# Performance work log

Measured on AMD Instinct MI355X. Metric: run time of the kernel, lower is better.

Reference implementation:

```python
import jax, jax.numpy as jnp
import numpy as np

B, A, NC, DIR, LMAX, MAXZ, NORB = 8, 64, 128, 4, 2, 10, 14
NF = NC * DIR * (2 * LMAX + 1)   # 2560
O2 = NORB * NORB                 # 196
AO = A * NORB                    # 896
LOG2 = float(np.log(2.0))

def ssp(v):  # spk shifted softplus
    return jax.nn.softplus(v) - LOG2

def setup_inputs():
    key = jax.random.key(0)
    ks = jax.random.split(key, 12)
    Z = jax.random.randint(ks[0], (B, A), 1, MAXZ)
    idx = np.arange(A)
    nbh_np = np.stack([np.delete(idx, i) for i in range(A)], 0)  # [A, A-1]: all atoms except self
    nbh = jnp.asarray(np.broadcast_to(nbh_np[None], (B, A, A - 1)).copy(), dtype=jnp.int32)
    x = jax.random.normal(ks[1], (B, A, NC), jnp.float32)
    Vijkl = jax.random.normal(ks[2], (B, A, A - 1, NF), jnp.float32) * 0.1
    sc = 1.0 / np.sqrt(NF)
    W_off = jax.random.normal(ks[3], (NF, O2), jnp.float32) * sc
    b_off = jnp.zeros((O2,), jnp.float32)
    W_on = jax.random.normal(ks[4], (NF, O2), jnp.float32) * sc
    b_on = jnp.zeros((O2,), jnp.float32)
    W_ovoff = jax.random.normal(ks[5], (NF, O2), jnp.float32) * sc
    b_ovoff = jnp.zeros((O2,), jnp.float32)
    ov_emb = jax.random.normal(ks[6], (MAXZ, O2), jnp.float32) * 0.1  # trainable overlap onsite embedding
    orb_energies = jax.random.normal(ks[7], (MAXZ, NORB), jnp.float32)  # h0 energies
    s0_energies = jnp.ones((MAXZ, NORB), jnp.float32)                   # s0 init = ones
    W1 = jax.random.normal(ks[8], (NC, NC // 2), jnp.float32) / np.sqrt(NC)
    b1 = jnp.zeros((NC // 2,), jnp.float32)
    W2 = jax.random.normal(ks[9], (NC // 2, 1), jnp.float32) / np.sqrt(NC // 2)
    b2 = jnp.zeros((1,), jnp.float32)
    return {"Z": Z, "nbh": nbh, "x": x, "Vijkl": Vijkl,
            "W_off": W_off, "b_off": b_off, "W_on": W_on, "b_on": b_on,
            "W_ovoff": W_ovoff, "b_ovoff": b_ovoff, "ov_emb": ov_emb,
            "orb_energies": orb_energies, "s0_energies": s0_energies,
            "W1": W1, "b1": b1, "W2": W2, "b2": b2}

def reference(Z, nbh, x, Vijkl, W_off, b_off, W_on, b_on, W_ovoff, b_ovoff,
              ov_emb, orb_energies, s0_energies, W1, b1, W2, b2):
    # permutation that reorders neighbor slots (plus appended zero/self slot) into atom order
    ar = jnp.broadcast_to(jnp.arange(A, dtype=nbh.dtype)[None, :, None], (B, A, 1))
    sort_idx = jnp.argsort(jnp.concatenate([nbh, ar], axis=2), axis=2)  # [B,A,A]
    eyeA = jnp.eye(A, dtype=Vijkl.dtype)
    eyeAO = jnp.eye(AO, dtype=Vijkl.dtype)

    def assemble(off, on):
        # off: [B,A,A-1,O2] pair blocks; on: [B,A,O2] onsite blocks
        offz = jnp.concatenate([off, jnp.zeros((B, A, 1, O2), off.dtype)], axis=2)  # zero self block at slot A-1
        offg = jnp.take_along_axis(offz, sort_idx[..., None], axis=2)               # [B,A,A,O2]
        M = offg + eyeA[None, :, :, None] * on[:, :, None, :]
        M = M.reshape(B, A, A, NORB, NORB).transpose(0, 1, 3, 2, 4).reshape(B, AO, AO)
        return 0.5 * (M + M.transpose(0, 2, 1))

    # Hamiltonian: offsite Dense + onsite Dense mean-aggregated over pairs
    H_off = Vijkl @ W_off + b_off                       # [B,A,A-1,O2]
    H_on = jnp.mean(Vijkl @ W_on + b_on, axis=2)        # [B,A,O2]
    H = assemble(H_off, H_on)
    # h0 single-atom diagonal (orb mask is all-active -> full diagonal)
    H = H + eyeAO[None] * orb_energies[Z].reshape(B, 1, AO)

    # Overlap: offsite Dense + onsite embedding lookup
    S_off = Vijkl @ W_ovoff + b_ovoff
    S_on = ov_emb[Z]                                    # [B,A,O2]
    S = assemble(S_off, S_on)
    S = S + eyeAO[None] * s0_energies[Z].reshape(B, 1, AO)

    # energy head: Dense->ssp->Dense->ScaleShift(0,1), sum over atoms
    Ei = ssp(x @ W1 + b1) @ W2 + b2                     # [B,A,1]
    E = jnp.sum(Ei, axis=1)                             # [B,1]
    return H, S, E
```

## Files before the change

### kernel.cpp

```cpp
#include <hip/hip_runtime.h>

#define B_      8
#define A_      64
#define NPAIR   63
#define NC_     128
#define NF_     2560
#define O2_     196
#define NORB_   14
#define AO_     896
#define NCOLS   588
#define CSTRIDE 640
#define KSTEPS  80
#define BM      64
#define BN      640
#define BSTEP_BYTES 40960

typedef short bf16x8 __attribute__((ext_vector_type(8)));
typedef float f32x4  __attribute__((ext_vector_type(4)));

__device__ __forceinline__ unsigned f2bf(float f) {
    unsigned u = __builtin_bit_cast(unsigned, f);
    return (u + 0x7fffu + ((u >> 16) & 1u)) >> 16;
}

__global__ __launch_bounds__(512)
void prep_energy(const float* __restrict__ W_off, const float* __restrict__ W_ovoff,
                 const float* __restrict__ W_on, unsigned short* __restrict__ Bws,
                 const float* __restrict__ x, const float* __restrict__ W1,
                 const float* __restrict__ b1, const float* __restrict__ W2,
                 const float* __restrict__ b2, float* __restrict__ E) {
    const int t = threadIdx.x;
    if (blockIdx.x < KSTEPS) {
        __shared__ float wt[32 * BN];
        const int ks = blockIdx.x;
        for (int e = t; e < 32 * BN; e += 512) {
            int kl = e / BN, c = e - kl * BN;
            int kg = ks * 32 + kl;
            float v = 0.f;
            if (c < O2_)          v = W_off  [(size_t)kg * O2_ + c];
            else if (c < 2 * O2_) v = W_ovoff[(size_t)kg * O2_ + (c - O2_)];
            else if (c < 3 * O2_) v = W_on   [(size_t)kg * O2_ + (c - 2 * O2_)];
            wt[kl * BN + c] = v;
        }
        __syncthreads();
        unsigned short* out = Bws + (size_t)ks * (BN * 32);
        for (int e = t; e < BN * 4; e += 512) {
            int n = e >> 2, sg = e & 3;
            uint4 w;
            w.x = f2bf(wt[(sg * 8 + 0) * BN + n]) | (f2bf(wt[(sg * 8 + 1) * BN + n]) << 16);
            w.y = f2bf(wt[(sg * 8 + 2) * BN + n]) | (f2bf(wt[(sg * 8 + 3) * BN + n]) << 16);
            w.z = f2bf(wt[(sg * 8 + 4) * BN + n]) | (f2bf(wt[(sg * 8 + 5) * BN + n]) << 16);
            w.w = f2bf(wt[(sg * 8 + 6) * BN + n]) | (f2bf(wt[(sg * 8 + 7) * BN + n]) << 16);
            *(uint4*)(out + (size_t)n * 32 + sg * 8) = w;
        }
    } else {
        __shared__ float partial[8];
        const int b = blockIdx.x - KSTEPS;
        const int lane = t & 63;
        const int w = t >> 6;
        float esum = 0.f;
        for (int aa = 0; aa < 8; ++aa) {
            const int a = w * 8 + aa;
            const float* xr = x + (size_t)(b * A_ + a) * NC_;
            float hj = b1[lane];
            for (int k = 0; k < NC_; ++k) hj = fmaf(xr[k], W1[k * 64 + lane], hj);
            float sp = fmaxf(hj, 0.f) + log1pf(expf(-fabsf(hj))) - 0.69314718055994531f;
            float v = sp * W2[lane];
            for (int off = 32; off; off >>= 1) v += __shfl_down(v, off);
            if (lane == 0) esum += v + b2[0];
        }
        if (lane == 0) partial[w] = esum;
        __syncthreads();
        if (t == 0) {
            float e = 0.f;
            for (int k = 0; k < 8; ++k) e += partial[k];
            E[b] = e;
        }
    }
}

__global__ __launch_bounds__(512, 4)
void gemm_off(const float* __restrict__ V, const unsigned short* __restrict__ Bws,
              const float* __restrict__ b_off, const float* __restrict__ b_ovoff,
              const float* __restrict__ b_on, float* __restrict__ HSoff) {
    __shared__ alignas(16) float Alds[2][BM * 32];

    const int tid  = threadIdx.x;
    int mtb = blockIdx.x;
    mtb = (mtb & 7) * 63 + (mtb >> 3);
    const int mt   = mtb;
    const int lane = tid & 63;
    const int wv   = tid >> 6;
    const int wvu  = __builtin_amdgcn_readfirstlane(wv);

    const int rr  = tid >> 3;
    const int sgp = (tid & 7) ^ (rr & 7);
    const float* asrc = V + (size_t)(mt * BM + rr) * NF_ + sgp * 4;

    const char* bp = (const char*)Bws + (size_t)(wv * 80 + (lane & 15)) * 64 + (lane >> 4) * 16;
#define BFRAG(t_, nf_) (*(const bf16x8*)(bp + (size_t)(t_) * BSTEP_BYTES + (nf_) * 1024))

    f32x4 acc[4][5];
#pragma unroll
    for (int mf = 0; mf < 4; ++mf)
#pragma unroll
        for (int nf = 0; nf < 5; ++nf)
            acc[mf][nf] = (f32x4){0.f, 0.f, 0.f, 0.f};

    auto stage = [&](int buf, int t) {
        __builtin_amdgcn_global_load_lds(
            (const __attribute__((address_space(1))) void*)(asrc + (size_t)t * 32),
            (__attribute__((address_space(3))) void*)(&Alds[buf][wvu * 256]), 16, 0, 0);
    };

    const unsigned klo = (unsigned)(lane >> 4) * 2;

    union U8 { unsigned u[4]; bf16x8 v; };

#define AFRAG(abf_, mf_, Abuf_) {                                                  \
    const unsigned R_ = (unsigned)(lane & 15) + (mf_) * 16;                        \
    const unsigned a0_ = R_ * 128 + ((klo ^ (R_ & 7)) << 4);                       \
    float4 lo_ = *(const float4*)((const char*)(Abuf_) + a0_);                     \
    float4 hi_ = *(const float4*)((const char*)(Abuf_) + (a0_ ^ 16));              \
    U8 uu_;                                                                        \
    asm("v_cvt_pk_bf16_f32 %0, %1, %2" : "=v"(uu_.u[0]) : "v"(lo_.x), "v"(lo_.y)); \
    asm("v_cvt_pk_bf16_f32 %0, %1, %2" : "=v"(uu_.u[1]) : "v"(lo_.z), "v"(lo_.w)); \
    asm("v_cvt_pk_bf16_f32 %0, %1, %2" : "=v"(uu_.u[2]) : "v"(hi_.x), "v"(hi_.y)); \
    asm("v_cvt_pk_bf16_f32 %0, %1, %2" : "=v"(uu_.u[3]) : "v"(hi_.z), "v"(hi_.w)); \
    abf_ = uu_.v; }

#define MFMA1(abf_, bq_, mf_, nf_) \
    acc[mf_][nf_] = __builtin_amdgcn_mfma_f32_16x16x32_bf16(abf_, bq_, acc[mf_][nf_], 0, 0, 0);

    bf16x8 bq0, bq1, bq2, bq3, bq4, abf;

    stage(0, 0);
    bq0 = BFRAG(0, 0); bq1 = BFRAG(0, 1); bq2 = BFRAG(0, 2); bq3 = BFRAG(0, 3); bq4 = BFRAG(0, 4);

    for (int t = 0; t < KSTEPS; ++t) {
        const int buf = t & 1;
        asm volatile("s_waitcnt vmcnt(5)" ::: "memory");
        __builtin_amdgcn_s_barrier();
        __builtin_amdgcn_sched_barrier(0);
        if (t + 1 < KSTEPS) stage(buf ^ 1, t + 1);

        const float* Abuf = &Alds[buf][0];
        AFRAG(abf, 0, Abuf);
        MFMA1(abf, bq0, 0, 0); MFMA1(abf, bq1, 0, 1); MFMA1(abf, bq2, 0, 2);
        MFMA1(abf, bq3, 0, 3); MFMA1(abf, bq4, 0, 4);
        AFRAG(abf, 1, Abuf);
        MFMA1(abf, bq0, 1, 0); MFMA1(abf, bq1, 1, 1); MFMA1(abf, bq2, 1, 2);
        MFMA1(abf, bq3, 1, 3); MFMA1(abf, bq4, 1, 4);
        AFRAG(abf, 2, Abuf);
        MFMA1(abf, bq0, 2, 0); MFMA1(abf, bq1, 2, 1); MFMA1(abf, bq2, 2, 2);
        MFMA1(abf, bq3, 2, 3); MFMA1(abf, bq4, 2, 4);
        AFRAG(abf, 3, Abuf);
        MFMA1(abf, bq0, 3, 0); bq0 = BFRAG(t + 1, 0);
        MFMA1(abf, bq1, 3, 1); bq1 = BFRAG(t + 1, 1);
        MFMA1(abf, bq2, 3, 2); bq2 = BFRAG(t + 1, 2);
        MFMA1(abf, bq3, 3, 3); bq3 = BFRAG(t + 1, 3);
        MFMA1(abf, bq4, 3, 4); bq4 = BFRAG(t + 1, 4);
        __builtin_amdgcn_sched_barrier(0);
    }

    const int c16 = lane & 15, rg = lane >> 4;
#pragma unroll
    for (int nf = 0; nf < 5; ++nf) {
        int C = wv * 80 + nf * 16 + c16;
        if (C >= NCOLS) continue;
        float bias = (C < O2_) ? b_off[C] : (C < 2 * O2_) ? b_ovoff[C - O2_] : b_on[C - 2 * O2_];
#pragma unroll
        for (int mf = 0; mf < 4; ++mf) {
            int R = mt * BM + mf * 16 + rg * 4;
            float* o = HSoff + (size_t)R * CSTRIDE + C;
            o[0]           = acc[mf][nf][0] + bias;
            o[CSTRIDE]     = acc[mf][nf][1] + bias;
            o[2 * CSTRIDE] = acc[mf][nf][2] + bias;
            o[3 * CSTRIDE] = acc[mf][nf][3] + bias;
        }
    }
#undef BFRAG
#undef AFRAG
#undef MFMA1
}

__global__ void hon_reduce(const float* __restrict__ HSoff, float* __restrict__ Hon) {
    const int g = blockIdx.x;
    const int t = threadIdx.x;
    if (t >= O2_) return;
    const float* p0 = HSoff + (size_t)g * NPAIR * CSTRIDE + 2 * O2_ + t;
    const float* p1 = p0 + (size_t)21 * CSTRIDE;
    const float* p2 = p0 + (size_t)42 * CSTRIDE;
    float a0 = 0.f, a1 = 0.f, a2 = 0.f;
#pragma unroll 3
    for (int j = 0; j < 21; ++j) {
        a0 += p0[0]; a1 += p1[0]; a2 += p2[0];
        p0 += CSTRIDE; p1 += CSTRIDE; p2 += CSTRIDE;
    }
    Hon[(size_t)g * O2_ + t] = (a0 + a1 + a2) * (1.f / (float)NPAIR);
}

__global__ __launch_bounds__(256)
void assemble_k(const float* __restrict__ HSoff, const float* __restrict__ Hon,
                const int* __restrict__ Z, const float* __restrict__ ov_emb,
                const float* __restrict__ orbE, const float* __restrict__ s0E,
                float* __restrict__ H, float* __restrict__ S) {
    __shared__ float Ai[NPAIR * 197];
    __shared__ float Bj[2][16 * 200];
    __shared__ float Dg[O2_];
    __shared__ float Dd[NORB_];

    const int bid = blockIdx.x;
    const int h = bid & 1, i = (bid >> 1) & 63, b = bid >> 7;
    const int t = threadIdx.x;
    const int g = b * A_ + i;
    const int z = Z[g];
    float* out = (h ? S : H) + (size_t)b * AO_ * AO_;

    const float* abase = HSoff + (size_t)g * NPAIR * CSTRIDE + h * O2_;
    for (int u = t; u < NPAIR * O2_; u += 256) {
        int jj = u / O2_, e = u - jj * O2_;
        Ai[jj * 197 + e] = abase[(size_t)jj * CSTRIDE + e];
    }
    if (t < O2_)   Dg[t] = h ? ov_emb[(size_t)z * O2_ + t]   : Hon[(size_t)g * O2_ + t];
    if (t < NORB_) Dd[t] = h ? s0E[(size_t)z * NORB_ + t]    : orbE[(size_t)z * NORB_ + t];

    auto stageB = [&](int buf, int jc) {
        for (int u = t; u < 16 * O2_; u += 256) {
            int jl = u / O2_, e = u - jl * O2_;
            int j = jc * 16 + jl;
            if (j != i) {
                int idx = (i < j) ? i : i - 1;
                Bj[buf][jl * 200 + e] =
                    HSoff[((size_t)(b * A_ + j) * NPAIR + idx) * CSTRIDE + h * O2_ + e];
            }
        }
    };
    stageB(0, 0);
    __syncthreads();

    const int tj = t / NORB_, tq = t - tj * NORB_;
    for (int jc = 0; jc < 4; ++jc) {
        if (jc < 3) stageB((jc + 1) & 1, jc + 1);
        if (t < 224) {
            const int j = jc * 16 + tj;
            const int cur = jc & 1;
#pragma unroll
            for (int p = 0; p < NORB_; ++p) {
                float v;
                if (j == i) {
                    v = 0.5f * (Dg[p * NORB_ + tq] + Dg[tq * NORB_ + p]);
                    if (p == tq) v += Dd[p];
                } else {
                    int jj = (j < i) ? j : j - 1;
                    v = 0.5f * (Ai[jj * 197 + p * NORB_ + tq] + Bj[cur][tj * 200 + tq * NORB_ + p]);
                }
                out[(size_t)(i * NORB_ + p) * AO_ + jc * 224 + t] = v;
            }
        }
        __syncthreads();
    }
}

extern "C" void kernel_launch(void* const* d_in, const int* in_sizes, int n_in,
                              void* d_out, int out_size, void* d_ws, size_t ws_size,
                              hipStream_t stream) {
    const int*   Z       = (const int*)  d_in[0];
    const float* x       = (const float*)d_in[2];
    const float* V       = (const float*)d_in[3];
    const float* W_off   = (const float*)d_in[4];
    const float* b_off   = (const float*)d_in[5];
    const float* W_on    = (const float*)d_in[6];
    const float* b_on    = (const float*)d_in[7];
    const float* W_ovoff = (const float*)d_in[8];
    const float* b_ovoff = (const float*)d_in[9];
    const float* ov_emb  = (const float*)d_in[10];
    const float* orbE    = (const float*)d_in[11];
    const float* s0E     = (const float*)d_in[12];
    const float* W1      = (const float*)d_in[13];
    const float* b1      = (const float*)d_in[14];
    const float* W2      = (const float*)d_in[15];
    const float* b2      = (const float*)d_in[16];

    float* H = (float*)d_out;
    float* S = H + (size_t)B_ * AO_ * AO_;
    float* E = S + (size_t)B_ * AO_ * AO_;

    char* ws = (char*)d_ws;
    unsigned short* Bws = (unsigned short*)ws;
    float* HSoff = (float*)(ws + (size_t)4  * 1024 * 1024);
    float* Hon   = (float*)(ws + (size_t)88 * 1024 * 1024);

    prep_energy<<<KSTEPS + B_, 512, 0, stream>>>(W_off, W_ovoff, W_on, Bws,
                                                 x, W1, b1, W2, b2, E);
    gemm_off   <<<504,  512, 0, stream>>>(V, Bws, b_off, b_ovoff, b_on, HSoff);
    hon_reduce <<<512,  256, 0, stream>>>(HSoff, Hon);
    assemble_k <<<1024, 256, 0, stream>>>(HSoff, Hon, Z, ov_emb, orbE, s0E, H, S);
}
```

Measured before the change: 265.9 us.

## Convert A tile to bf16 once per block in LDS before MFMA

Instead of every wave converting fp32 A fragments to bf16 on each read (8 waves each redoing the conversion), each thread converts one float4 of the staged tile into a separate bf16 LDS buffer with a new swizzle. MFMA fragments then come from a single 16-byte bf16 LDS load. The change adds an extra barrier and an lgkmcnt wait per k-step, plus more LDS use. It also wraps the MFMA groups in s_setprio to favour matrix issue.

```diff
diff --git a/kernel.cpp b/kernel.cpp
--- a/kernel.cpp
+++ b/kernel.cpp
@@ -83,7 +83,8 @@
 void gemm_off(const float* __restrict__ V, const unsigned short* __restrict__ Bws,
               const float* __restrict__ b_off, const float* __restrict__ b_ovoff,
               const float* __restrict__ b_on, float* __restrict__ HSoff) {
-    __shared__ alignas(16) float Alds[2][BM * 32];
+    __shared__ alignas(16) float          Af32[2][BM * 32];
+    __shared__ alignas(16) unsigned short Ab16[2][BM * 32];
 
     const int tid  = threadIdx.x;
     int mtb = blockIdx.x;
@@ -93,9 +94,7 @@
     const int wv   = tid >> 6;
     const int wvu  = __builtin_amdgcn_readfirstlane(wv);
 
-    const int rr  = tid >> 3;
-    const int sgp = (tid & 7) ^ (rr & 7);
-    const float* asrc = V + (size_t)(mt * BM + rr) * NF_ + sgp * 4;
+    const float* asrc = V + (size_t)(mt * BM + (tid >> 3)) * NF_ + (tid & 7) * 4;
 
     const char* bp = (const char*)Bws + (size_t)(wv * 80 + (lane & 15)) * 64 + (lane >> 4) * 16;
 #define BFRAG(t_, nf_) (*(const bf16x8*)(bp + (size_t)(t_) * BSTEP_BYTES + (nf_) * 1024))
@@ -110,24 +109,20 @@
     auto stage = [&](int buf, int t) {
         __builtin_amdgcn_global_load_lds(
             (const __attribute__((address_space(1))) void*)(asrc + (size_t)t * 32),
-            (__attribute__((address_space(3))) void*)(&Alds[buf][wvu * 256]), 16, 0, 0);
+            (__attribute__((address_space(3))) void*)(&Af32[buf][wvu * 256]), 16, 0, 0);
     };
 
-    const unsigned klo = (unsigned)(lane >> 4) * 2;
-
-    union U8 { unsigned u[4]; bf16x8 v; };
-
-#define AFRAG(abf_, mf_, Abuf_) {                                                  \
-    const unsigned R_ = (unsigned)(lane & 15) + (mf_) * 16;                        \
-    const unsigned a0_ = R_ * 128 + ((klo ^ (R_ & 7)) << 4);                       \
-    float4 lo_ = *(const float4*)((const char*)(Abuf_) + a0_);                     \
-    float4 hi_ = *(const float4*)((const char*)(Abuf_) + (a0_ ^ 16));              \
-    U8 uu_;                                                                        \
-    asm("v_cvt_pk_bf16_f32 %0, %1, %2" : "=v"(uu_.u[0]) : "v"(lo_.x), "v"(lo_.y)); \
-    asm("v_cvt_pk_bf16_f32 %0, %1, %2" : "=v"(uu_.u[1]) : "v"(lo_.z), "v"(lo_.w)); \
-    asm("v_cvt_pk_bf16_f32 %0, %1, %2" : "=v"(uu_.u[2]) : "v"(hi_.x), "v"(hi_.y)); \
-    asm("v_cvt_pk_bf16_f32 %0, %1, %2" : "=v"(uu_.u[3]) : "v"(hi_.z), "v"(hi_.w)); \
-    abf_ = uu_.v; }
+    const int crr = tid >> 3, cq = tid & 7;
+    const int csl = ((cq >> 1) + ((crr + (crr >> 2)) & 3)) & 3;
+    char* const cdst_base0 = (char*)&Ab16[0][0] + crr * 64 + csl * 16 + (cq & 1) * 8;
+    char* const cdst_base1 = (char*)&Ab16[1][0] + crr * 64 + csl * 16 + (cq & 1) * 8;
+
+    const unsigned klo4 = (unsigned)(lane >> 4);
+
+#define AFRAG(abf_, mf_, Bb16_) {                                                   \
+    const unsigned R_ = (unsigned)(lane & 15) + (mf_) * 16;                         \
+    const unsigned sl_ = (klo4 + ((R_ + (R_ >> 2)) & 3)) & 3;                       \
+    abf_ = *(const bf16x8*)((const char*)(Bb16_) + R_ * 64 + sl_ * 16); }
 
 #define MFMA1(abf_, bq_, mf_, nf_) \
     acc[mf_][nf_] = __builtin_amdgcn_mfma_f32_16x16x32_bf16(abf_, bq_, acc[mf_][nf_], 0, 0, 0);
@@ -140,26 +135,48 @@
     for (int t = 0; t < KSTEPS; ++t) {
         const int buf = t & 1;
         asm volatile("s_waitcnt vmcnt(5)" ::: "memory");
+        __builtin_amdgcn_sched_barrier(0);
         __builtin_amdgcn_s_barrier();
         __builtin_amdgcn_sched_barrier(0);
         if (t + 1 < KSTEPS) stage(buf ^ 1, t + 1);
 
-        const float* Abuf = &Alds[buf][0];
-        AFRAG(abf, 0, Abuf);
+        {
+            float4 cf = *(const float4*)((const char*)&Af32[buf][0] + tid * 16);
+            unsigned lo, hi;
+            asm("v_cvt_pk_bf16_f32 %0, %1, %2" : "=v"(lo) : "v"(cf.x), "v"(cf.y));
+            asm("v_cvt_pk_bf16_f32 %0, %1, %2" : "=v"(hi) : "v"(cf.z), "v"(cf.w));
+            uint2 cw = {lo, hi};
+            *(uint2*)(buf ? cdst_base1 : cdst_base0) = cw;
+        }
+        asm volatile("s_waitcnt lgkmcnt(0)" ::: "memory");
+        __builtin_amdgcn_sched_barrier(0);
+        __builtin_amdgcn_s_barrier();
+        __builtin_amdgcn_sched_barrier(0);
+
+        const unsigned short* At = &Ab16[buf][0];
+        AFRAG(abf, 0, At);
+        __builtin_amdgcn_s_setprio(1);
         MFMA1(abf, bq0, 0, 0); MFMA1(abf, bq1, 0, 1); MFMA1(abf, bq2, 0, 2);
         MFMA1(abf, bq3, 0, 3); MFMA1(abf, bq4, 0, 4);
-        AFRAG(abf, 1, Abuf);
+        __builtin_amdgcn_s_setprio(0);
+        AFRAG(abf, 1, At);
+        __builtin_amdgcn_s_setprio(1);
         MFMA1(abf, bq0, 1, 0); MFMA1(abf, bq1, 1, 1); MFMA1(abf, bq2, 1, 2);
         MFMA1(abf, bq3, 1, 3); MFMA1(abf, bq4, 1, 4);
-        AFRAG(abf, 2, Abuf);
+        __builtin_amdgcn_s_setprio(0);
+        AFRAG(abf, 2, At);
+        __builtin_amdgcn_s_setprio(1);
         MFMA1(abf, bq0, 2, 0); MFMA1(abf, bq1, 2, 1); MFMA1(abf, bq2, 2, 2);
         MFMA1(abf, bq3, 2, 3); MFMA1(abf, bq4, 2, 4);
-        AFRAG(abf, 3, Abuf);
+        __builtin_amdgcn_s_setprio(0);
+        AFRAG(abf, 3, At);
+        __builtin_amdgcn_s_setprio(1);
         MFMA1(abf, bq0, 3, 0); bq0 = BFRAG(t + 1, 0);
         MFMA1(abf, bq1, 3, 1); bq1 = BFRAG(t + 1, 1);
         MFMA1(abf, bq2, 3, 2); bq2 = BFRAG(t + 1, 2);
         MFMA1(abf, bq3, 3, 3); bq3 = BFRAG(t + 1, 3);
         MFMA1(abf, bq4, 3, 4); bq4 = BFRAG(t + 1, 4);
+        __builtin_amdgcn_s_setprio(0);
         __builtin_amdgcn_sched_barrier(0);
     }
 
```

New measurement: 263.7 us. Within noise of the previous version (-0.8%).
